# Kernel tuning notes

Hardware: AMD Instinct MI355X
Metric: run time of the kernel (lower is better)

Reference implementation:

```python
import jax, jax.numpy as jnp
import numpy as np

N_NODES = 50000
N_EDGES = 400000
HID = 64
NUM_REL = 230
NUM_TS = 365
SLOPE = 0.2  # LeakyReLU negative slope

def lrelu(v):
    return jnp.where(v >= 0, v, SLOPE * v)

def setup_inputs() -> dict:
    key = jax.random.key(0)
    ks = jax.random.split(key, 10)
    x = jax.random.normal(ks[0], (N_NODES, 2 * HID), dtype=jnp.float32)
    rel_table = jax.random.normal(ks[1], (NUM_REL, HID), dtype=jnp.float32) * 0.1
    time_table = jax.random.normal(ks[2], (NUM_TS, HID), dtype=jnp.float32) * 0.1
    W_rt = jax.random.normal(ks[3], (2 * HID, 2 * HID), dtype=jnp.float32) * (1.0 / np.sqrt(2 * HID))
    b_rt = jnp.zeros((2 * HID,), dtype=jnp.float32)
    W_fc = jax.random.normal(ks[4], (6 * HID, 2 * HID), dtype=jnp.float32) * (1.0 / np.sqrt(6 * HID))
    b_fc = jnp.zeros((2 * HID,), dtype=jnp.float32)
    src = jax.random.randint(ks[5], (N_EDGES,), 0, N_NODES)
    dst = jax.random.randint(ks[6], (N_EDGES,), 0, N_NODES)
    rel = jax.random.randint(ks[7], (N_EDGES,), 0, NUM_REL)
    ts = jax.random.randint(ks[8], (N_EDGES,), 0, NUM_TS)
    edges = jnp.stack([src, dst, rel, ts], axis=1).astype(jnp.int64) if jax.config.jax_enable_x64 else jnp.stack([src, dst, rel, ts], axis=1)
    return {
        "x": x, "rel_table": rel_table, "time_table": time_table,
        "W_rt": W_rt, "b_rt": b_rt, "W_fc": W_fc, "b_fc": b_fc,
        "edges": edges, "num_nodes": N_NODES,
    }

def reference(x, rel_table, time_table, W_rt, b_rt, W_fc, b_fc, edges, num_nodes):
    # MessagePassing.forward + LogicalGNN.aggregated_messages (scatter_mean)
    src, dst, rel, ts = edges[:, 0], edges[:, 1], edges[:, 2], edges[:, 3]
    rel_e = rel_table[rel]          # [E, H]
    time_e = time_table[ts]         # [E, H]
    rel_t = lrelu(jnp.concatenate([rel_e, time_e], axis=-1) @ W_rt + b_rt)  # [E, 2H]
    msg_in = jnp.concatenate([x[src], rel_t, x[dst]], axis=-1)              # [E, 6H]
    messages = lrelu(msg_in @ W_fc + b_fc)                                  # [E, 2H]
    # scatter_mean over dst
    sums = jax.ops.segment_sum(messages, dst, num_segments=num_nodes)       # [N, 2H]
    counts = jax.ops.segment_sum(jnp.ones((messages.shape[0],), messages.dtype), dst, num_segments=num_nodes)
    agg = sums / jnp.maximum(counts, 1.0)[:, None]
    return agg
```

## Files before the change

### kernel.cpp

```cpp
#include <hip/hip_runtime.h>
#include <cstdio>

#define HID 64
#define D 128
#define NUM_REL 230
#define NUM_TS 365
#define NCOMB (NUM_REL*NUM_TS)
#define SLOPE 0.2f
#define XPAD 136
#define MAXDEG 64

typedef __attribute__((ext_vector_type(8))) short short8;
typedef __attribute__((ext_vector_type(4))) float f32x4;

__device__ __forceinline__ float lrelu(float v){ return v >= 0.f ? v : SLOPE*v; }

__device__ __forceinline__ unsigned bf_rne(float f){
    unsigned u = __float_as_uint(f);
    return (u + 0x7fffu + ((u >> 16) & 1u)) >> 16;
}
__device__ __forceinline__ unsigned pk2(float a, float b){
    return bf_rne(a) | (bf_rne(b) << 16);
}
__device__ __forceinline__ float bf_lo(unsigned u){ return __uint_as_float(u << 16); }
__device__ __forceinline__ float bf_hi(unsigned u){ return __uint_as_float(u & 0xffff0000u); }

__global__ __launch_bounds__(256) void k_prep(
        const float* __restrict__ rel_table, const float* __restrict__ time_table,
        const float* __restrict__ W_rt, const float* __restrict__ W_fc,
        float* __restrict__ relP, float* __restrict__ timP,
        unsigned short* __restrict__ Wpk13, unsigned short* __restrict__ Wpk2)
{
    int b = blockIdx.x;
    if (b < 298) {
        int row = b*2 + (threadIdx.x >> 7);
        int j   = threadIdx.x & 127;
        if (row >= NUM_REL + NUM_TS) return;
        const float* tbl; const float* Wb; float* out;
        if (row < NUM_REL) { tbl = rel_table + row*HID;            Wb = W_rt;          out = relP + row*D; }
        else               { tbl = time_table + (row-NUM_REL)*HID; Wb = W_rt + HID*D;  out = timP + (row-NUM_REL)*D; }
        float acc = 0.f;
        #pragma unroll
        for (int k = 0; k < HID; ++k) acc += tbl[k] * Wb[k*D + j];
        out[j] = acc;
    } else {
        int id = (b - 298)*256 + threadIdx.x;
        if (id < 4096) {
            int mt = id >> 8;
            int s  = (id >> 6) & 3;
            int l  = id & 63;
            int m  = mt*16 + (l & 15);
            int kb = s*32 + (l >> 4)*8;
            unsigned short* dst = Wpk13 + ((size_t)(mt*4 + s)*64 + l)*8;
            #pragma unroll
            for (int j = 0; j < 8; ++j) {
                int k = kb + j;
                float v = (m < D) ? W_fc[(size_t)k*D + m]
                                  : W_fc[(size_t)(256 + k)*D + (m - D)];
                dst[j] = (unsigned short)bf_rne(v);
            }
        } else {
            int id2 = id - 4096;
            int mt = id2 >> 8;
            int s  = (id2 >> 6) & 3;
            int l  = id2 & 63;
            int m  = mt*16 + (l & 15);
            int kb = s*32 + (l >> 4)*8;
            unsigned short* dst = Wpk2 + ((size_t)(mt*4 + s)*64 + l)*8;
            #pragma unroll
            for (int j = 0; j < 8; ++j) {
                int k = kb + j;
                dst[j] = (unsigned short)bf_rne(W_fc[(size_t)(D + k)*D + m]);
            }
        }
    }
}

__device__ __forceinline__ void xw_body(
        int xb, const float* __restrict__ x,
        const unsigned short* __restrict__ Wpk13,
        unsigned short* __restrict__ xW13bf, int n_nodes,
        unsigned short* Xs )
{
    int t = threadIdx.x;
    int nodeBase = xb*64;
    {
        int row = t >> 2;
        int k0  = (t & 3)*32;
        int node = nodeBase + row;
        unsigned short* dst = Xs + row*XPAD + k0;
        if (node < n_nodes) {
            const float4* src = (const float4*)(x + (size_t)node*D + k0);
            #pragma unroll
            for (int g = 0; g < 8; ++g) {
                float4 v = src[g];
                *(uint2*)(dst + g*4) = make_uint2(pk2(v.x, v.y), pk2(v.z, v.w));
            }
        } else {
            #pragma unroll
            for (int g = 0; g < 8; ++g)
                *(uint2*)(dst + g*4) = make_uint2(0u, 0u);
        }
    }
    __syncthreads();

    int w = t >> 6, l = t & 63;
    int li = l & 15, q = l >> 4;

    f32x4 acc[4][4];
    #pragma unroll
    for (int mi = 0; mi < 4; ++mi)
        #pragma unroll
        for (int ni = 0; ni < 4; ++ni) acc[mi][ni] = (f32x4){0.f,0.f,0.f,0.f};

    #pragma unroll 1
    for (int s = 0; s < 4; ++s) {
        short8 af[4], bf[4];
        #pragma unroll
        for (int mi = 0; mi < 4; ++mi) {
            int mt = w*4 + mi;
            af[mi] = *(const short8*)(Wpk13 + ((size_t)(mt*4 + s)*64 + l)*8);
        }
        #pragma unroll
        for (int ni = 0; ni < 4; ++ni)
            bf[ni] = *(const short8*)(Xs + (ni*16 + li)*XPAD + s*32 + q*8);
        #pragma unroll
        for (int mi = 0; mi < 4; ++mi)
            #pragma unroll
            for (int ni = 0; ni < 4; ++ni)
                acc[mi][ni] = __builtin_amdgcn_mfma_f32_16x16x32_bf16(
                                  af[mi], bf[ni], acc[mi][ni], 0, 0, 0);
    }
    #pragma unroll
    for (int ni = 0; ni < 4; ++ni) {
        int node = nodeBase + ni*16 + li;
        if (node >= n_nodes) continue;
        #pragma unroll
        for (int mi = 0; mi < 4; ++mi) {
            int col = w*64 + mi*16 + q*4;
            *(uint2*)(xW13bf + (size_t)node*256 + col) =
                make_uint2(pk2(acc[mi][ni][0], acc[mi][ni][1]),
                           pk2(acc[mi][ni][2], acc[mi][ni][3]));
        }
    }
}

__device__ __forceinline__ void t2_body(
        int tb, const float* __restrict__ relP, const float* __restrict__ timP,
        const float* __restrict__ b_rt, const unsigned short* __restrict__ Wpk2,
        unsigned short* __restrict__ T2bf,
        unsigned short* Hs )
{
    int t = threadIdx.x;
    int cBase = tb*128;
    {
        int r  = t >> 1;
        int hk = (t & 1)*64;
        int combo = cBase + r;
        if (combo >= NCOMB) combo = NCOMB - 1;
        int rr = combo / NUM_TS;
        int tt = combo - rr*NUM_TS;
        const float4* rv4 = (const float4*)(relP + (size_t)rr*D + hk);
        const float4* tv4 = (const float4*)(timP + (size_t)tt*D + hk);
        const float4* bv4 = (const float4*)(b_rt + hk);
        unsigned short* dst = Hs + r*XPAD + hk;
        #pragma unroll
        for (int g = 0; g < 16; ++g) {
            float4 rv = rv4[g], tv = tv4[g], bv = bv4[g];
            float v0 = lrelu(rv.x+tv.x+bv.x), v1 = lrelu(rv.y+tv.y+bv.y);
            float v2 = lrelu(rv.z+tv.z+bv.z), v3 = lrelu(rv.w+tv.w+bv.w);
            *(uint2*)(dst + g*4) = make_uint2(pk2(v0,v1), pk2(v2,v3));
        }
    }
    __syncthreads();

    int w = t >> 6, l = t & 63;
    int li = l & 15, q = l >> 4;
    int mb = (w & 1)*4;
    int nb = (w >> 1)*64;

    f32x4 acc[4][4];
    #pragma unroll
    for (int mi = 0; mi < 4; ++mi)
        #pragma unroll
        for (int ni = 0; ni < 4; ++ni) acc[mi][ni] = (f32x4){0.f,0.f,0.f,0.f};

    #pragma unroll 1
    for (int s = 0; s < 4; ++s) {
        short8 af[4], bf[4];
        #pragma unroll
        for (int mi = 0; mi < 4; ++mi)
            af[mi] = *(const short8*)(Wpk2 + ((size_t)((mb+mi)*4 + s)*64 + l)*8);
        #pragma unroll
        for (int ni = 0; ni < 4; ++ni)
            bf[ni] = *(const short8*)(Hs + (nb + ni*16 + li)*XPAD + s*32 + q*8);
        #pragma unroll
        for (int mi = 0; mi < 4; ++mi)
            #pragma unroll
            for (int ni = 0; ni < 4; ++ni)
                acc[mi][ni] = __builtin_amdgcn_mfma_f32_16x16x32_bf16(
                                  af[mi], bf[ni], acc[mi][ni], 0, 0, 0);
    }
    #pragma unroll
    for (int ni = 0; ni < 4; ++ni) {
        int combo = cBase + nb + ni*16 + li;
        if (combo >= NCOMB) continue;
        #pragma unroll
        for (int mi = 0; mi < 4; ++mi) {
            int col = (mb + mi)*16 + q*4;
            *(uint2*)(T2bf + (size_t)combo*D + col) =
                make_uint2(pk2(acc[mi][ni][0], acc[mi][ni][1]),
                           pk2(acc[mi][ni][2], acc[mi][ni][3]));
        }
    }
}

__global__ __launch_bounds__(256, 3) void k_mm(
        const float* __restrict__ x, const unsigned short* __restrict__ Wpk13,
        unsigned short* __restrict__ xW13bf, int n_nodes,
        const float* __restrict__ relP, const float* __restrict__ timP,
        const float* __restrict__ b_rt, const unsigned short* __restrict__ Wpk2,
        unsigned short* __restrict__ T2bf,
        const int* __restrict__ edges, int n_edges,
        int* __restrict__ deg, int2* __restrict__ ebuf,
        int nsc, int nxw)
{
    __shared__ __align__(16) unsigned short Hs[128*XPAD];
    int b = blockIdx.x;
    if (b < nsc) {
        int e = b*256 + threadIdx.x;
        if (e < n_edges) {
            int4 ed = ((const int4*)edges)[e];
            int slot = atomicAdd(&deg[ed.y], 1);
            if (slot < MAXDEG)
                ebuf[(size_t)ed.y*MAXDEG + slot] = make_int2(ed.x, ed.z*NUM_TS + ed.w);
        }
    } else if (b < nsc + nxw) {
        xw_body(b - nsc, x, Wpk13, xW13bf, n_nodes, Hs);
    } else {
        t2_body(b - nsc - nxw, relP, timP, b_rt, Wpk2, T2bf, Hs);
    }
}

__global__ __launch_bounds__(256) void k_agg(
        const int* __restrict__ deg, const int2* __restrict__ ebuf,
        const unsigned short* __restrict__ xW13bf,
        const unsigned short* __restrict__ T2bf,
        const float* __restrict__ b_fc,
        float* __restrict__ out, int n_nodes)
{
    int t    = threadIdx.x;
    int lane = t & 63;
    int g    = lane >> 4;
    int sub  = lane & 15;
    int node = blockIdx.x*16 + (t >> 6)*4 + g;
    bool valid = node < n_nodes;
    int nodeC  = valid ? node : n_nodes - 1;

    int dg  = deg[nodeC];
    int cnt = valid ? (dg < MAXDEG ? dg : MAXDEG) : 0;
    int cm1 = cnt > 0 ? cnt - 1 : 0;
    const int2* eb = ebuf + (size_t)nodeC * MAXDEG;

    int cmax = cnt;
    cmax = max(cmax, __shfl_xor(cmax, 16));
    cmax = max(cmax, __shfl_xor(cmax, 32));

    float base[8];
    {
        uint4  w3  = *(const uint4*)&xW13bf[(size_t)nodeC*256 + 128 + sub*8];
        float4 blo = *(const float4*)&b_fc[sub*8];
        float4 bhi = *(const float4*)&b_fc[sub*8 + 4];
        base[0] = bf_lo(w3.x) + blo.x; base[1] = bf_hi(w3.x) + blo.y;
        base[2] = bf_lo(w3.y) + blo.z; base[3] = bf_hi(w3.y) + blo.w;
        base[4] = bf_lo(w3.z) + bhi.x; base[5] = bf_hi(w3.z) + bhi.y;
        base[6] = bf_lo(w3.w) + bhi.z; base[7] = bf_hi(w3.w) + bhi.w;
    }

    float acc[8];
    #pragma unroll
    for (int k = 0; k < 8; ++k) acc[k] = 0.f;

    const unsigned sMax = (unsigned)(n_nodes - 1);
    const unsigned cMax = (unsigned)(NCOMB - 1);

    for (int e = 0; e < cmax; e += 4) {
        int2 e0 = eb[min(e + 0, cm1)];
        int2 e1 = eb[min(e + 1, cm1)];
        int2 e2 = eb[min(e + 2, cm1)];
        int2 e3 = eb[min(e + 3, cm1)];
        unsigned s0 = min((unsigned)e0.x, sMax), c0 = min((unsigned)e0.y, cMax);
        unsigned s1 = min((unsigned)e1.x, sMax), c1 = min((unsigned)e1.y, cMax);
        unsigned s2 = min((unsigned)e2.x, sMax), c2 = min((unsigned)e2.y, cMax);
        unsigned s3 = min((unsigned)e3.x, sMax), c3 = min((unsigned)e3.y, cMax);
        uint4 S0 = *(const uint4*)&xW13bf[(size_t)s0*256 + sub*8];
        uint4 T0 = *(const uint4*)&T2bf  [(size_t)c0*D   + sub*8];
        uint4 S1 = *(const uint4*)&xW13bf[(size_t)s1*256 + sub*8];
        uint4 T1 = *(const uint4*)&T2bf  [(size_t)c1*D   + sub*8];
        uint4 S2 = *(const uint4*)&xW13bf[(size_t)s2*256 + sub*8];
        uint4 T2 = *(const uint4*)&T2bf  [(size_t)c2*D   + sub*8];
        uint4 S3 = *(const uint4*)&xW13bf[(size_t)s3*256 + sub*8];
        uint4 T3 = *(const uint4*)&T2bf  [(size_t)c3*D   + sub*8];
        bool m0 = (e + 0) < cnt, m1 = (e + 1) < cnt;
        bool m2 = (e + 2) < cnt, m3 = (e + 3) < cnt;
        #pragma unroll
        for (int w = 0; w < 4; ++w) {
            unsigned Sw0 = (&S0.x)[w], Tw0 = (&T0.x)[w];
            unsigned Sw1 = (&S1.x)[w], Tw1 = (&T1.x)[w];
            unsigned Sw2 = (&S2.x)[w], Tw2 = (&T2.x)[w];
            unsigned Sw3 = (&S3.x)[w], Tw3 = (&T3.x)[w];
            float v0l = lrelu(bf_lo(Sw0) + bf_lo(Tw0) + base[2*w]);
            float v0h = lrelu(bf_hi(Sw0) + bf_hi(Tw0) + base[2*w+1]);
            float v1l = lrelu(bf_lo(Sw1) + bf_lo(Tw1) + base[2*w]);
            float v1h = lrelu(bf_hi(Sw1) + bf_hi(Tw1) + base[2*w+1]);
            float v2l = lrelu(bf_lo(Sw2) + bf_lo(Tw2) + base[2*w]);
            float v2h = lrelu(bf_hi(Sw2) + bf_hi(Tw2) + base[2*w+1]);
            float v3l = lrelu(bf_lo(Sw3) + bf_lo(Tw3) + base[2*w]);
            float v3h = lrelu(bf_hi(Sw3) + bf_hi(Tw3) + base[2*w+1]);
            float a01l = (m0 ? v0l : 0.f) + (m1 ? v1l : 0.f);
            float a23l = (m2 ? v2l : 0.f) + (m3 ? v3l : 0.f);
            float a01h = (m0 ? v0h : 0.f) + (m1 ? v1h : 0.f);
            float a23h = (m2 ? v2h : 0.f) + (m3 ? v3h : 0.f);
            acc[2*w]   += a01l + a23l;
            acc[2*w+1] += a01h + a23h;
        }
    }

    if (!valid) return;
    float inv = 1.f / fmaxf((float)dg, 1.f);
    float4 o0 = make_float4(acc[0]*inv, acc[1]*inv, acc[2]*inv, acc[3]*inv);
    float4 o1 = make_float4(acc[4]*inv, acc[5]*inv, acc[6]*inv, acc[7]*inv);
    *(float4*)&out[(size_t)node*D + sub*8]     = o0;
    *(float4*)&out[(size_t)node*D + sub*8 + 4] = o1;
}

extern "C" void kernel_launch(void* const* d_in, const int* in_sizes, int n_in,
                              void* d_out, int out_size, void* d_ws, size_t ws_size,
                              hipStream_t stream)
{
    const float* x          = (const float*)d_in[0];
    const float* rel_table  = (const float*)d_in[1];
    const float* time_table = (const float*)d_in[2];
    const float* W_rt       = (const float*)d_in[3];
    const float* b_rt       = (const float*)d_in[4];
    const float* W_fc       = (const float*)d_in[5];
    const float* b_fc       = (const float*)d_in[6];
    const int*   edges      = (const int*)d_in[7];

    int n_nodes = in_sizes[0] / D;
    int n_edges = in_sizes[7] / 4;
    int nblkE   = (n_edges + 255) / 256;
    int nxw     = (n_nodes + 63) / 64;
    int nt2     = (NCOMB + 127) / 128;

    char* ws = (char*)d_ws;
    size_t off = 0;
    auto alloc = [&](size_t bytes) -> void* {
        void* p = ws + off; off += (bytes + 255) & ~(size_t)255; return p;
    };
    unsigned short* xW13bf = (unsigned short*)alloc((size_t)n_nodes * 256 * 2);
    unsigned short* T2bf   = (unsigned short*)alloc((size_t)NCOMB * D * 2);
    unsigned short* Wpk13  = (unsigned short*)alloc((size_t)16*4*64*8 * 2);
    unsigned short* Wpk2   = (unsigned short*)alloc((size_t)8*4*64*8 * 2);
    float* relP   = (float*)alloc((size_t)NUM_REL * D * sizeof(float));
    float* timP   = (float*)alloc((size_t)NUM_TS * D * sizeof(float));
    int*   deg    = (int*)alloc((size_t)n_nodes * sizeof(int));
    int2*  ebuf   = (int2*)alloc((size_t)n_nodes * MAXDEG * sizeof(int2));
    if (off > ws_size)
        fprintf(stderr, "kernel_launch: workspace too small: need %zu, have %zu\n", off, ws_size);

    hipMemsetAsync(deg, 0, (size_t)n_nodes * sizeof(int), stream);

    k_prep<<<322, 256, 0, stream>>>(rel_table, time_table, W_rt, W_fc,
                                    relP, timP, Wpk13, Wpk2);
    k_mm  <<<nblkE + nxw + nt2, 256, 0, stream>>>(x, Wpk13, xW13bf, n_nodes,
                                                  relP, timP, b_rt, Wpk2, T2bf,
                                                  edges, n_edges, deg, ebuf,
                                                  nblkE, nxw);
    k_agg <<<(n_nodes + 15)/16, 256, 0, stream>>>(deg, ebuf, xW13bf, T2bf,
                                                  b_fc, (float*)d_out, n_nodes);
}
```

Before: 177.6 us.

## Interleave scatter blocks with GEMM blocks and halve T2 tile size

The fused k_mm kernel now spreads the edge-scatter blocks evenly among the matmul blocks using a proportional index mapping, so atomics and MFMA work run concurrently instead of in separate phases of the grid. The T2 precompute tile drops from 128 to 64 combos per block, which halves shared memory (more resident blocks) and doubles the block count. In exchange each block does less MFMA work per weight-fragment load, and there is extra integer division per block for the mapping.

```diff
diff --git a/kernel.cpp b/kernel.cpp
--- a/kernel.cpp
+++ b/kernel.cpp
@@ -152,10 +152,10 @@
         unsigned short* Hs )
 {
     int t = threadIdx.x;
-    int cBase = tb*128;
+    int cBase = tb*64;
     {
-        int r  = t >> 1;
-        int hk = (t & 1)*64;
+        int r  = t >> 2;
+        int hk = (t & 3)*32;
         int combo = cBase + r;
         if (combo >= NCOMB) combo = NCOMB - 1;
         int rr = combo / NUM_TS;
@@ -165,7 +165,7 @@
         const float4* bv4 = (const float4*)(b_rt + hk);
         unsigned short* dst = Hs + r*XPAD + hk;
         #pragma unroll
-        for (int g = 0; g < 16; ++g) {
+        for (int g = 0; g < 8; ++g) {
             float4 rv = rv4[g], tv = tv4[g], bv = bv4[g];
             float v0 = lrelu(rv.x+tv.x+bv.x), v1 = lrelu(rv.y+tv.y+bv.y);
             float v2 = lrelu(rv.z+tv.z+bv.z), v3 = lrelu(rv.w+tv.w+bv.w);
@@ -176,26 +176,26 @@
 
     int w = t >> 6, l = t & 63;
     int li = l & 15, q = l >> 4;
-    int mb = (w & 1)*4;
-    int nb = (w >> 1)*64;
-
-    f32x4 acc[4][4];
-    #pragma unroll
-    for (int mi = 0; mi < 4; ++mi)
+
+    f32x4 acc[2][4];
+    #pragma unroll
+    for (int mi = 0; mi < 2; ++mi)
         #pragma unroll
         for (int ni = 0; ni < 4; ++ni) acc[mi][ni] = (f32x4){0.f,0.f,0.f,0.f};
 
     #pragma unroll 1
     for (int s = 0; s < 4; ++s) {
-        short8 af[4], bf[4];
-        #pragma unroll
-        for (int mi = 0; mi < 4; ++mi)
-            af[mi] = *(const short8*)(Wpk2 + ((size_t)((mb+mi)*4 + s)*64 + l)*8);
+        short8 af[2], bf[4];
+        #pragma unroll
+        for (int mi = 0; mi < 2; ++mi) {
+            int mt = w*2 + mi;
+            af[mi] = *(const short8*)(Wpk2 + ((size_t)(mt*4 + s)*64 + l)*8);
+        }
         #pragma unroll
         for (int ni = 0; ni < 4; ++ni)
-            bf[ni] = *(const short8*)(Hs + (nb + ni*16 + li)*XPAD + s*32 + q*8);
-        #pragma unroll
-        for (int mi = 0; mi < 4; ++mi)
+            bf[ni] = *(const short8*)(Hs + (ni*16 + li)*XPAD + s*32 + q*8);
+        #pragma unroll
+        for (int mi = 0; mi < 2; ++mi)
             #pragma unroll
             for (int ni = 0; ni < 4; ++ni)
                 acc[mi][ni] = __builtin_amdgcn_mfma_f32_16x16x32_bf16(
@@ -203,11 +203,11 @@
     }
     #pragma unroll
     for (int ni = 0; ni < 4; ++ni) {
-        int combo = cBase + nb + ni*16 + li;
+        int combo = cBase + ni*16 + li;
         if (combo >= NCOMB) continue;
         #pragma unroll
-        for (int mi = 0; mi < 4; ++mi) {
-            int col = (mb + mi)*16 + q*4;
+        for (int mi = 0; mi < 2; ++mi) {
+            int col = (w*2 + mi)*16 + q*4;
             *(uint2*)(T2bf + (size_t)combo*D + col) =
                 make_uint2(pk2(acc[mi][ni][0], acc[mi][ni][1]),
                            pk2(acc[mi][ni][2], acc[mi][ni][3]));
@@ -223,22 +223,27 @@
         unsigned short* __restrict__ T2bf,
         const int* __restrict__ edges, int n_edges,
         int* __restrict__ deg, int2* __restrict__ ebuf,
-        int nsc, int nxw)
-{
-    __shared__ __align__(16) unsigned short Hs[128*XPAD];
+        int nsc, int nxw, int ntot)
+{
+    __shared__ __align__(16) unsigned short Hs[64*XPAD];
     int b = blockIdx.x;
-    if (b < nsc) {
-        int e = b*256 + threadIdx.x;
+    int cumCur  = (int)(((long long)b       * nsc) / ntot);
+    int cumNext = (int)(((long long)(b + 1) * nsc) / ntot);
+    if (cumNext > cumCur) {
+        int e = cumCur*256 + threadIdx.x;
         if (e < n_edges) {
             int4 ed = ((const int4*)edges)[e];
             int slot = atomicAdd(&deg[ed.y], 1);
             if (slot < MAXDEG)
                 ebuf[(size_t)ed.y*MAXDEG + slot] = make_int2(ed.x, ed.z*NUM_TS + ed.w);
         }
-    } else if (b < nsc + nxw) {
-        xw_body(b - nsc, x, Wpk13, xW13bf, n_nodes, Hs);
     } else {
-        t2_body(b - nsc - nxw, relP, timP, b_rt, Wpk2, T2bf, Hs);
+        int cidx = b - cumNext;
+        if (cidx < nxw) {
+            xw_body(cidx, x, Wpk13, xW13bf, n_nodes, Hs);
+        } else {
+            t2_body(cidx - nxw, relP, timP, b_rt, Wpk2, T2bf, Hs);
+        }
     }
 }
 
@@ -351,7 +356,8 @@
     int n_edges = in_sizes[7] / 4;
     int nblkE   = (n_edges + 255) / 256;
     int nxw     = (n_nodes + 63) / 64;
-    int nt2     = (NCOMB + 127) / 128;
+    int nt2     = (NCOMB + 63) / 64;
+    int ntot    = nblkE + nxw + nt2;
 
     char* ws = (char*)d_ws;
     size_t off = 0;
@@ -373,10 +379,10 @@
 
     k_prep<<<322, 256, 0, stream>>>(rel_table, time_table, W_rt, W_fc,
                                     relP, timP, Wpk13, Wpk2);
-    k_mm  <<<nblkE + nxw + nt2, 256, 0, stream>>>(x, Wpk13, xW13bf, n_nodes,
-                                                  relP, timP, b_rt, Wpk2, T2bf,
-                                                  edges, n_edges, deg, ebuf,
-                                                  nblkE, nxw);
+    k_mm  <<<ntot, 256, 0, stream>>>(x, Wpk13, xW13bf, n_nodes,
+                                     relP, timP, b_rt, Wpk2, T2bf,
+                                     edges, n_edges, deg, ebuf,
+                                     nblkE, nxw, ntot);
     k_agg <<<(n_nodes + 15)/16, 256, 0, stream>>>(deg, ebuf, xW13bf, T2bf,
                                                   b_fc, (float*)d_out, n_nodes);
 }
```

New measurement: 169.9 us. -4.3%, faster.
